# Performance work log

Measured on AMD Instinct MI355X. Metric: run time of the kernel, lower is better.

## Reference

```python
import jax, jax.numpy as jnp
import numpy as np

B, H, W, D, L, M = 16, 256, 256, 32, 4, 12  # batch, grid H, grid W, d_model, num_layers, modes
BN_EPS = 1e-5


def setup_inputs() -> dict:
    key = jax.random.key(0)
    ks = jax.random.split(key, 12)
    scale = 1.0 / (D * D)  # SpectralConv2d init scale: 1/(in_ch*out_ch)
    return {
        "x": jax.random.normal(ks[0], (B, H, W), jnp.float32),
        "coords_x": jax.random.uniform(ks[1], (1, 2, 1, H, W), dtype=jnp.float32),
        # linear_in: 3 -> D
        "w_in": jax.random.normal(ks[2], (D, 3), jnp.float32) * 0.3,
        "b_in": jnp.zeros((D,), jnp.float32),
        # per-layer spectral weights (real/imag), torch.rand-style uniform [0,1)*scale
        "w1r": jax.random.uniform(ks[3], (L, D, D, M, M), dtype=jnp.float32) * scale,
        "w1i": jax.random.uniform(ks[4], (L, D, D, M, M), dtype=jnp.float32) * scale,
        "w2r": jax.random.uniform(ks[5], (L, D, D, M, M), dtype=jnp.float32) * scale,
        "w2i": jax.random.uniform(ks[6], (L, D, D, M, M), dtype=jnp.float32) * scale,
        # per-layer pointwise linear D -> D
        "lw": jax.random.normal(ks[7], (L, D, D), jnp.float32) * (1.0 / np.sqrt(D)),
        "lb": jnp.zeros((L, D), jnp.float32),
        # per-layer BatchNorm affine params
        "gamma": jnp.ones((L, D), jnp.float32),
        "beta": jnp.zeros((L, D), jnp.float32),
        # linear_out: D -> 1
        "w_out": jax.random.normal(ks[8], (1, D), jnp.float32) * (1.0 / np.sqrt(D)),
        "b_out": jnp.zeros((1,), jnp.float32),
    }


def _fourier_layer(h, w1, w2, lw, lb, gamma, beta):
    # h: [B, D, H, W]
    Bh, C, Hh, Wh = h.shape
    h_ft = jnp.fft.rfft2(h)  # [B, D, H, W//2+1] complex64
    # low-mode truncation + complex channel mixing on two corner blocks
    top = jnp.einsum('bixy,ioxy->boxy', h_ft[:, :, :M, :M], w1)
    bot = jnp.einsum('bixy,ioxy->boxy', h_ft[:, :, Hh - M:, :M], w2)
    out_ft = jnp.zeros((Bh, C, Hh, Wh // 2 + 1), jnp.complex64)
    out_ft = out_ft.at[:, :, :M, :M].set(top).at[:, :, Hh - M:, :M].set(bot)
    y = jnp.fft.irfft2(out_ft, s=(Hh, Wh))  # [B, D, H, W]
    # residual pointwise linear (x + Linear(x)), then ReLU, then BatchNorm2d (batch stats)
    y = y + jnp.einsum('bchw,oc->bohw', y, lw) + lb[None, :, None, None]
    y = jax.nn.relu(y)
    mean = y.mean(axis=(0, 2, 3), keepdims=True)
    var = y.var(axis=(0, 2, 3), keepdims=True)
    y = (y - mean) * jax.lax.rsqrt(var + BN_EPS)
    return y * gamma[None, :, None, None] + beta[None, :, None, None]


def reference(x, coords_x, w_in, b_in, w1r, w1i, w2r, w2i, lw, lb, gamma, beta, w_out, b_out):
    # coords_x: [1,2,1,H,W] -> squeeze dim 2 -> broadcast to [B,2,H,W]
    cx = jnp.broadcast_to(coords_x[:, :, 0], (x.shape[0], 2, H, W))
    h = jnp.concatenate([x[:, None], cx], axis=1)  # [B, 3, H, W]
    h = jnp.einsum('bchw,dc->bdhw', h, w_in) + b_in[None, :, None, None]  # linear_in
    for i in range(L):  # fixed small layer count
        h = _fourier_layer(h, w1r[i] + 1j * w1i[i], w2r[i] + 1j * w2i[i],
                           lw[i], lb[i], gamma[i], beta[i])
    out = jnp.einsum('bdhw,od->bohw', h, w_out) + b_out[None, :, None, None]  # linear_out
    return out[:, 0]  # [B, H, W]
```

## Files before the change

kernel.cpp:

```cpp
#include <hip/hip_runtime.h>

constexpr double PI2 = 6.283185307179586476925286766559;
constexpr float INV_HW = 1.0f / 65536.0f;


__global__ __launch_bounds__(256) void k_init(float* __restrict__ cs,
                                              float* __restrict__ Tg) {
  int t = threadIdx.x;
  double a = PI2 * (double)t / 256.0;
  cs[2*t]   = (float)cos(a);
  cs[2*t+1] = (float)sin(a);
  for (int i = t; i < 1536; i += 256) {
    int k = i >> 7, xs = i & 127;
    double ang = PI2 * (double)(k * xs) / 256.0;
    Tg[i]        = (float)cos(ang);
    Tg[1536 + i] = (float)sin(ang);
  }
}

__global__ __launch_bounds__(256) void k_prep(
    const float* __restrict__ w1r, const float* __restrict__ w1i,
    const float* __restrict__ w2r, const float* __restrict__ w2i,
    const float* __restrict__ lw, float* __restrict__ wf)
{
  const int bid = blockIdx.x;
  const int l = bid / 288, m = bid % 288;
  const int ky = m / 12, kx = m % 12;
  const int kyp = (ky < 12) ? ky : ky - 12;
  const float* wr_ = ((ky < 12) ? w1r : w2r) + l*147456;
  const float* wi_ = ((ky < 12) ? w1i : w2i) + l*147456;
  __shared__ float wre[1024], wim[1024], lwl[1024];
  const int tid = threadIdx.x;
  for (int f = tid; f < 1024; f += 256) {
    int idx = f*144 + kyp*12 + kx;
    wre[f] = wr_[idx]; wim[f] = wi_[idx];
    lwl[f] = lw[l*1024 + f];
  }
  __syncthreads();
  float* o_ = wf + (long)bid*2048;
  for (int f = tid; f < 1024; f += 256) {
    int i = f >> 5, o = f & 31;
    float ar = wre[f], ai = wim[f];
    #pragma unroll
    for (int c = 0; c < 32; ++c) {
      float lv = lwl[o*32 + c];
      ar += wre[i*32 + c] * lv;
      ai += wim[i*32 + c] * lv;
    }
    o_[f] = ar; o_[1024 + f] = ai;
  }
}

__global__ __launch_bounds__(256) void k_embed_fwd(
    const float* __restrict__ xin, const float* __restrict__ coords,
    const float* __restrict__ w_in, const float* __restrict__ b_in,
    const float* __restrict__ Tg, float* __restrict__ gxo)
{
  __shared__ float wl[96], bl[32];
  __shared__ __align__(16) float Tl[3168];
  __shared__ __align__(16) float E[32*132];
  __shared__ __align__(16) float O[32*132];
  const int tid = threadIdx.x;
  if (tid < 96) wl[tid] = w_in[tid];
  if (tid >= 96 && tid < 128) bl[tid-96] = b_in[tid-96];
  for (int i = tid; i < 1536; i += 256) {
    int k = i >> 7, xs0 = i & 127;
    Tl[k*132 + xs0]        = Tg[i];
    Tl[1584 + k*132 + xs0] = Tg[1536 + i];
  }
  const int b = blockIdx.x >> 8, y = blockIdx.x & 255;
  const int xs = tid & 127, half = tid >> 7;
  const int cbase = half << 4;
  const int xhi = (256 - xs) & 255;
  const float xvL = xin[(b*256 + y)*256 + xs];
  const float c0L = coords[y*256 + xs];
  const float c1L = coords[65536 + y*256 + xs];
  const float xvH = xin[(b*256 + y)*256 + xhi];
  const float c0H = coords[y*256 + xhi];
  const float c1H = coords[65536 + y*256 + xhi];
  __syncthreads();
  #pragma unroll
  for (int cc = 0; cc < 16; ++cc) {
    const int c = cbase + cc;
    float lo = wl[3*c]*xvL + wl[3*c+1]*c0L + wl[3*c+2]*c1L + bl[c];
    float hi = wl[3*c]*xvH + wl[3*c+1]*c0H + wl[3*c+2]*c1H + bl[c];
    E[c*132 + xs] = (xs == 0) ? lo : (lo + hi);
    O[c*132 + xs] = (xs == 0) ? 0.f : (lo - hi);
  }
  if (tid < 32) {
    const int c = tid;
    const float xv = xin[(b*256 + y)*256 + 128];
    const float c0 = coords[y*256 + 128];
    const float c1 = coords[65536 + y*256 + 128];
    E[c*132 + 128] = wl[3*c]*xv + wl[3*c+1]*c0 + wl[3*c+2]*c1 + bl[c];
  }
  __syncthreads();
  const int wv = tid >> 6, lane = tid & 63;
  const int seg = lane >> 3, chl = lane & 7;
  const int ch = wv*8 + chl;
  float ar[12], ai[12];
  #pragma unroll
  for (int k = 0; k < 12; ++k) { ar[k] = 0.f; ai[k] = 0.f; }
  {
    const float* Erow = &E[ch*132 + seg*16];
    const float* Orow = &O[ch*132 + seg*16];
    #pragma unroll
    for (int c4 = 0; c4 < 4; ++c4) {
      float4 E4 = *(const float4*)(Erow + 4*c4);
      float4 O4 = *(const float4*)(Orow + 4*c4);
      ar[0] += E4.x + E4.y + E4.z + E4.w;
      #pragma unroll
      for (int k = 1; k < 12; ++k) {
        float4 Tc4 = *(const float4*)&Tl[k*132 + seg*16 + 4*c4];
        float4 Ts4 = *(const float4*)&Tl[1584 + k*132 + seg*16 + 4*c4];
        ar[k] += E4.x*Tc4.x + E4.y*Tc4.y + E4.z*Tc4.z + E4.w*Tc4.w;
        ai[k] -= O4.x*Ts4.x + O4.y*Ts4.y + O4.z*Ts4.z + O4.w*Ts4.w;
      }
    }
  }
  #pragma unroll
  for (int k = 0; k < 12; ++k) {
    ar[k] += __shfl_xor(ar[k], 8, 64);
    ar[k] += __shfl_xor(ar[k], 16, 64);
    ar[k] += __shfl_xor(ar[k], 32, 64);
  }
  #pragma unroll
  for (int k = 1; k < 12; ++k) {
    ai[k] += __shfl_xor(ai[k], 8, 64);
    ai[k] += __shfl_xor(ai[k], 16, 64);
    ai[k] += __shfl_xor(ai[k], 32, 64);
  }
  {
    const float e128 = E[ch*132 + 128];
    float* gp = gxo + ((long)(b*256 + y)*32 + ch)*24;
    #pragma unroll
    for (int j = 0; j < 3; ++j) {
      const int v = seg*3 + j;
      if (v < 12) {
        float s = ar[v] + ((v & 1) ? -e128 : e128);
        gp[2*v] = s;
        if (v == 0) gp[1] = 0.f;
      } else if (v < 23) {
        gp[2*(v - 11) + 1] = ai[v - 11];
      }
    }
  }
}

__global__ __launch_bounds__(512) void k_spec(
    const float* __restrict__ gx, const float* __restrict__ cs,
    const float* __restrict__ bnp, const float* __restrict__ wfl,
    float* __restrict__ gy)
{
  const int bid = (blockIdx.x % 8) * 24 + blockIdx.x / 8;
  const int b = bid / 12, kx = bid % 12;
  __shared__ float2 Z[32*257];
  __shared__ float fcl[24*66];
  __shared__ float fml[24*66];
  __shared__ __align__(16) float csl[512];
  const int tid = threadIdx.x;
  if (tid < 512) csl[tid] = cs[tid];
  {
    const int ch = tid & 31;
    float sc = 1.0f, badd = 0.0f;
    if (bnp) { sc = bnp[ch]; if (kx == 0) badd = 256.0f * bnp[32 + ch]; }
    const float* src = gx + ((long)(b*256)*32 + ch)*24 + 2*kx;
    const int ybase = tid >> 5;
    #pragma unroll
    for (int i = 0; i < 16; ++i) {
      int y = ybase + 16*i;
      float2 v = *(const float2*)(src + (long)y*768);
      float2 w; w.x = sc*v.x + badd; w.y = sc*v.y;
      Z[ch*257 + y] = w;
    }
  }
  __syncthreads();
  for (int t = tid; t < 832; t += 512) {
    const int hf = t & 1, r = t >> 1;
    const int pr = r % 13, ch = r / 13;
    const int kyv = (pr <= 10) ? (pr + 1) : ((pr == 11) ? 0 : 244);
    const int y0 = hf << 7;
    int tt = (kyv * y0) & 255;
    float A = 0.f, Bv = 0.f, C2 = 0.f, D = 0.f;
    const float2* Zp = &Z[ch*257 + y0];
    for (int i = 0; i < 128; ++i) {
      float2 v = Zp[i];
      float2 w = *(const float2*)&csl[2*tt];
      A  += v.x*w.x;  D  += v.x*w.y;
      C2 += v.y*w.x;  Bv += v.y*w.y;
      tt = (tt + kyv) & 255;
    }
    A  += __shfl_xor(A, 1, 64);
    Bv += __shfl_xor(Bv, 1, 64);
    C2 += __shfl_xor(C2, 1, 64);
    D  += __shfl_xor(D, 1, 64);
    if (hf == 0) {
      const int slo = (pr <= 10) ? (pr + 1) : ((pr == 11) ? 0 : 12);
      fcl[slo*66 + 2*ch]     = A + Bv;
      fcl[slo*66 + 2*ch + 1] = C2 - D;
      if (pr <= 10) {
        fcl[(23 - pr)*66 + 2*ch]     = A - Bv;
        fcl[(23 - pr)*66 + 2*ch + 1] = C2 + D;
      }
    }
  }
  __syncthreads();
  for (int t = tid; t < 768; t += 512) {
    const int ky = t >> 5, o = t & 31;
    const float* wb = wfl + ((long)(ky*12 + kx))*2048;
    const float* fr = &fcl[ky*66];
    float ar = 0.f, ai = 0.f;
    #pragma unroll
    for (int i = 0; i < 32; ++i) {
      float fre = fr[2*i], fim = fr[2*i+1];
      float wr = wb[i*32 + o], wi = wb[1024 + i*32 + o];
      ar += fre*wr - fim*wi;
      ai += fre*wi + fim*wr;
    }
    fml[ky*66 + 2*o]     = ar;
    fml[ky*66 + 2*o + 1] = ai;
  }
  __syncthreads();
  {
    const int yp = tid & 127, og = tid >> 7;
    float tc[24], tsn[24];
    #pragma unroll
    for (int s = 0; s < 24; ++s) {
      int kyv = (s < 12) ? s : (232 + s);
      int tt = (kyv * yp) & 255;
      tc[s] = csl[2*tt]; tsn[s] = csl[2*tt+1];
    }
    const int yhi = (256 - yp) & 255;
    float* rowLo = gy + ((long)(b*256 + yp))*768 + kx*64;
    float* rowHi = gy + ((long)(b*256 + yhi))*768 + kx*64;
    #pragma unroll
    for (int oo = 0; oo < 8; oo += 2) {
      const int o = og*8 + oo;
      float A1a=0.f,A2a=0.f,A3a=0.f,A4a=0.f;
      float A1b=0.f,A2b=0.f,A3b=0.f,A4b=0.f;
      #pragma unroll
      for (int s = 0; s < 24; ++s) {
        float fra = fml[s*66 + 2*o],     fia = fml[s*66 + 2*o + 1];
        float frb = fml[s*66 + 2*o + 2], fib = fml[s*66 + 2*o + 3];
        float c = tc[s], sn = tsn[s];
        A1a += fra*c;  A2a += fia*sn;  A3a += fra*sn;  A4a += fia*c;
        A1b += frb*c;  A2b += fib*sn;  A3b += frb*sn;  A4b += fib*c;
      }
      float4 lo, hi;
      lo.x = (A1a - A2a)*INV_HW; lo.y = (A3a + A4a)*INV_HW;
      lo.z = (A1b - A2b)*INV_HW; lo.w = (A3b + A4b)*INV_HW;
      hi.x = (A1a + A2a)*INV_HW; hi.y = (A4a - A3a)*INV_HW;
      hi.z = (A1b + A2b)*INV_HW; hi.w = (A4b - A3b)*INV_HW;
      *(float4*)(rowLo + 2*o) = lo;
      *(float4*)(rowHi + 2*o) = hi;
    }
  }
  if (tid < 32) {
    const int o = tid;
    float re = 0.f, im = 0.f;
    #pragma unroll
    for (int s = 0; s < 24; ++s) {
      float fr = fml[s*66 + 2*o], fi = fml[s*66 + 2*o + 1];
      if (s & 1) { re -= fr; im -= fi; } else { re += fr; im += fi; }
    }
    float* row = gy + ((long)(b*256 + 128))*768 + kx*64;
    row[2*o]     = re*INV_HW;
    row[2*o + 1] = im*INV_HW;
  }
}

__global__ __launch_bounds__(256) void k_fuse(
    const float* __restrict__ gy, const float* __restrict__ Tg,
    const float* __restrict__ lb,
    float* __restrict__ gxo, float* __restrict__ part, float* __restrict__ z)
{
  const int b = blockIdx.x >> 8, y = blockIdx.x & 255;
  const int tid = threadIdx.x;
  __shared__ __align__(16) float Tl[3168];
  __shared__ __align__(16) float E[32*132];
  __shared__ __align__(16) float O[32*132];
  for (int i = tid; i < 1536; i += 256) {
    int k = i >> 7, xs0 = i & 127;
    Tl[k*132 + xs0]        = Tg[i];
    Tl[1584 + k*132 + xs0] = Tg[1536 + i];
  }
  const int xs = tid & 127, half = tid >> 7;
  const int cbase = half << 4;
  const int xhi = (256 - xs) & 255;
  float tc[12], tsn[12];
  #pragma unroll
  for (int kx = 1; kx < 12; ++kx) {
    tc[kx]  = 2.0f * Tg[kx*128 + xs];
    tsn[kx] = 2.0f * Tg[1536 + kx*128 + xs];
  }
  const float* Gg = gy + (long)(b*256 + y)*768;
  float zlo[16], zhi[16];
  #pragma unroll
  for (int cc = 0; cc < 16; cc += 2) {
    const int c = cbase + cc;
    float base0 = Gg[2*c], base1 = Gg[2*c + 2];
    float cos0 = 0.f, sin0 = 0.f, cos1 = 0.f, sin1 = 0.f;
    #pragma unroll
    for (int kx = 1; kx < 12; ++kx) {
      float4 g = *(const float4*)(Gg + kx*64 + 2*c);
      cos0 += g.x*tc[kx];  sin0 += g.y*tsn[kx];
      cos1 += g.z*tc[kx];  sin1 += g.w*tsn[kx];
    }
    const float l0 = lb[c], l1 = lb[c+1];
    zlo[cc]   = fmaxf(base0 + cos0 - sin0 + l0, 0.f);
    zhi[cc]   = fmaxf(base0 + cos0 + sin0 + l0, 0.f);
    zlo[cc+1] = fmaxf(base1 + cos1 - sin1 + l1, 0.f);
    zhi[cc+1] = fmaxf(base1 + cos1 + sin1 + l1, 0.f);
  }
  #pragma unroll
  for (int cc = 0; cc < 16; ++cc) {
    float e = (xs == 0) ? zlo[cc] : (zlo[cc] + zhi[cc]);
    float o = (xs == 0) ? 0.f     : (zlo[cc] - zhi[cc]);
    E[(cbase+cc)*132 + xs] = e;
    O[(cbase+cc)*132 + xs] = o;
  }
  if (z) {
    #pragma unroll
    for (int cc = 0; cc < 16; ++cc) {
      z[((b*32 + cbase+cc)*256 + y)*256 + xs]  = zlo[cc];
      z[((b*32 + cbase+cc)*256 + y)*256 + xhi] = zhi[cc];
    }
  }
  if (tid < 32) {
    const int c = tid;
    float acc = Gg[2*c] + lb[c];
    #pragma unroll
    for (int kx = 1; kx < 12; ++kx) {
      float2 g = *(const float2*)(Gg + kx*64 + 2*c);
      acc += (kx & 1) ? (-2.0f * g.x) : (2.0f * g.x);
    }
    float zv = fmaxf(acc, 0.f);
    E[c*132 + 128] = zv;
    if (z) z[((b*32 + c)*256 + y)*256 + 128] = zv;
  }
  __syncthreads();
  const int wv = tid >> 6, lane = tid & 63;
  const int seg = lane >> 3, chl = lane & 7;
  const int ch = wv*8 + chl;
  float ar[12], ai[12], sq = 0.f;
  #pragma unroll
  for (int k = 0; k < 12; ++k) { ar[k] = 0.f; ai[k] = 0.f; }
  {
    const float* Erow = &E[ch*132 + seg*16];
    const float* Orow = &O[ch*132 + seg*16];
    if (gxo) {
      #pragma unroll
      for (int c4 = 0; c4 < 4; ++c4) {
        float4 E4 = *(const float4*)(Erow + 4*c4);
        float4 O4 = *(const float4*)(Orow + 4*c4);
        ar[0] += E4.x + E4.y + E4.z + E4.w;
        #pragma unroll
        for (int k = 1; k < 12; ++k) {
          float4 Tc4 = *(const float4*)&Tl[k*132 + seg*16 + 4*c4];
          float4 Ts4 = *(const float4*)&Tl[1584 + k*132 + seg*16 + 4*c4];
          ar[k] += E4.x*Tc4.x + E4.y*Tc4.y + E4.z*Tc4.z + E4.w*Tc4.w;
          ai[k] -= O4.x*Ts4.x + O4.y*Ts4.y + O4.z*Ts4.z + O4.w*Ts4.w;
        }
        sq += E4.x*E4.x + E4.y*E4.y + E4.z*E4.z + E4.w*E4.w
            + O4.x*O4.x + O4.y*O4.y + O4.z*O4.z + O4.w*O4.w;
      }
    } else {
      #pragma unroll
      for (int c4 = 0; c4 < 4; ++c4) {
        float4 E4 = *(const float4*)(Erow + 4*c4);
        float4 O4 = *(const float4*)(Orow + 4*c4);
        ar[0] += E4.x + E4.y + E4.z + E4.w;
        sq += E4.x*E4.x + E4.y*E4.y + E4.z*E4.z + E4.w*E4.w
            + O4.x*O4.x + O4.y*O4.y + O4.z*O4.z + O4.w*O4.w;
      }
    }
  }
  #pragma unroll
  for (int k = 0; k < 12; ++k) {
    ar[k] += __shfl_xor(ar[k], 8, 64);
    ar[k] += __shfl_xor(ar[k], 16, 64);
    ar[k] += __shfl_xor(ar[k], 32, 64);
  }
  if (gxo) {
    #pragma unroll
    for (int k = 1; k < 12; ++k) {
      ai[k] += __shfl_xor(ai[k], 8, 64);
      ai[k] += __shfl_xor(ai[k], 16, 64);
      ai[k] += __shfl_xor(ai[k], 32, 64);
    }
  }
  sq += __shfl_xor(sq, 8, 64);
  sq += __shfl_xor(sq, 16, 64);
  sq += __shfl_xor(sq, 32, 64);
  {
    const float e0   = E[ch*132];
    const float e128 = E[ch*132 + 128];
    float* gp = gxo ? (gxo + ((long)(b*256 + y)*32 + ch)*24) : nullptr;
    #pragma unroll
    for (int j = 0; j < 3; ++j) {
      const int v = seg*3 + j;
      if (v < 12) {
        float s = ar[v] + ((v & 1) ? -e128 : e128);
        if (gp) {
          gp[2*v] = s;
          if (v == 0) gp[1] = 0.f;
        }
        if (v == 0) part[(long)blockIdx.x*64 + 2*ch] = s;
      } else if (v < 23) {
        if (gp) gp[2*(v - 11) + 1] = ai[v - 11];
      } else {
        part[(long)blockIdx.x*64 + 2*ch + 1] = 0.5f*sq + 0.5f*e0*e0 + e128*e128;
      }
    }
  }
}

__global__ __launch_bounds__(256) void k_stats(
    const float* __restrict__ part, const float* __restrict__ gamma,
    const float* __restrict__ beta, float* __restrict__ bn)
{
  const int c = blockIdx.x, tid = threadIdx.x;
  float s1 = 0.f, s2 = 0.f;
  for (int j = tid; j < 4096; j += 256) {
    s1 += part[(long)j*64 + 2*c];
    s2 += part[(long)j*64 + 2*c + 1];
  }
  #pragma unroll
  for (int d = 32; d; d >>= 1) {
    s1 += __shfl_xor(s1, d, 64);
    s2 += __shfl_xor(s2, d, 64);
  }
  __shared__ float r1[4], r2[4];
  int w = tid >> 6;
  if ((tid & 63) == 0) { r1[w] = s1; r2[w] = s2; }
  __syncthreads();
  if (tid == 0) {
    float S1 = r1[0]+r1[1]+r1[2]+r1[3];
    float S2 = r2[0]+r2[1]+r2[2]+r2[3];
    const float N = 1048576.0f;
    float mean = S1 / N;
    float var  = S2 / N - mean*mean;
    float inv  = rsqrtf(var + 1e-5f);
    float sc   = gamma[c] * inv;
    bn[c]      = sc;
    bn[32 + c] = beta[c] - mean*sc;
  }
}

__global__ __launch_bounds__(256) void k_out(
    const float* __restrict__ z, const float* __restrict__ bn,
    const float* __restrict__ w_out, const float* __restrict__ b_out,
    float* __restrict__ out)
{
  __shared__ float a[32];
  __shared__ float c0s;
  const int tid = threadIdx.x;
  if (tid < 32) a[tid] = bn[tid] * w_out[tid];
  if (tid == 0) {
    float t = b_out[0];
    for (int c = 0; c < 32; ++c) t += bn[32 + c] * w_out[c];
    c0s = t;
  }
  __syncthreads();
  int gid = blockIdx.x*256 + tid;
  int b = gid >> 14, pos = (gid & 16383) << 2;
  const float* zb = z + (long)b*2097152 + pos;
  float c0 = c0s;
  float r0 = c0, r1 = c0, r2 = c0, r3 = c0;
  #pragma unroll 8
  for (int c = 0; c < 32; ++c) {
    float4 v = *(const float4*)(zb + c*65536);
    float ac = a[c];
    r0 += v.x*ac; r1 += v.y*ac; r2 += v.z*ac; r3 += v.w*ac;
  }
  float4 res; res.x = r0; res.y = r1; res.z = r2; res.w = r3;
  *(float4*)(out + (long)b*65536 + pos) = res;
}

extern "C" void kernel_launch(void* const* d_in, const int* in_sizes, int n_in,
                              void* d_out, int out_size, void* d_ws, size_t ws_size,
                              hipStream_t stream) {
  const float* x      = (const float*)d_in[0];
  const float* coords = (const float*)d_in[1];
  const float* w_in   = (const float*)d_in[2];
  const float* b_in   = (const float*)d_in[3];
  const float* w1r    = (const float*)d_in[4];
  const float* w1i    = (const float*)d_in[5];
  const float* w2r    = (const float*)d_in[6];
  const float* w2i    = (const float*)d_in[7];
  const float* lw     = (const float*)d_in[8];
  const float* lb     = (const float*)d_in[9];
  const float* gamma  = (const float*)d_in[10];
  const float* beta   = (const float*)d_in[11];
  const float* w_out  = (const float*)d_in[12];
  const float* b_out  = (const float*)d_in[13];
  float* out = (float*)d_out;
  float* ws  = (float*)d_ws;

  float* cs   = ws;
  float* z    = cs + 512;
  float* gx   = z;
  float* wf   = z + 3145728;
  float* gy   = z + 33554432;
  float* part = gy + 3145728;
  float* Tg   = part + 294912;
  float* bn   = Tg + 294912;

  k_init<<<1, 256, 0, stream>>>(cs, Tg);
  k_prep<<<1152, 256, 0, stream>>>(w1r, w1i, w2r, w2i, lw, wf);
  k_embed_fwd<<<4096, 256, 0, stream>>>(x, coords, w_in, b_in, Tg, gx);

  for (int l = 0; l < 4; ++l) {
    k_spec<<<192, 512, 0, stream>>>(gx, cs, (l == 0) ? nullptr : bn,
                                    wf + (long)l*589824, gy);
    k_fuse<<<4096, 256, 0, stream>>>(gy, Tg, lb + l*32,
                                     (l < 3) ? gx : nullptr, part,
                                     (l == 3) ? z : nullptr);
    k_stats<<<32, 256, 0, stream>>>(part, gamma + l*32, beta + l*32, bn);
  }

  k_out<<<1024, 256, 0, stream>>>(z, bn, w_out, b_out, out);
}
```

Before: 544.3 us.

## Factor the per-segment DFT twiddles and drop the shared twiddle table in k_fuse

```diff
diff --git a/kernel.cpp b/kernel.cpp
--- a/kernel.cpp
+++ b/kernel.cpp
@@ -15,6 +15,12 @@
     double ang = PI2 * (double)(k * xs) / 256.0;
     Tg[i]        = (float)cos(ang);
     Tg[1536 + i] = (float)sin(ang);
+  }
+  for (int i = t; i < 176; i += 256) {
+    int k = (i >> 4) + 1, j = i & 15;
+    double ang = PI2 * (double)(k * j) / 256.0;
+    Tg[3072 + i] = (float)cos(ang);
+    Tg[3248 + i] = (float)sin(ang);
   }
 }
 
@@ -276,14 +282,8 @@
 {
   const int b = blockIdx.x >> 8, y = blockIdx.x & 255;
   const int tid = threadIdx.x;
-  __shared__ __align__(16) float Tl[3168];
   __shared__ __align__(16) float E[32*132];
   __shared__ __align__(16) float O[32*132];
-  for (int i = tid; i < 1536; i += 256) {
-    int k = i >> 7, xs0 = i & 127;
-    Tl[k*132 + xs0]        = Tg[i];
-    Tl[1584 + k*132 + xs0] = Tg[1536 + i];
-  }
   const int xs = tid & 127, half = tid >> 7;
   const int cbase = half << 4;
   const int xhi = (256 - xs) & 255;
@@ -342,51 +342,71 @@
   const int wv = tid >> 6, lane = tid & 63;
   const int seg = lane >> 3, chl = lane & 7;
   const int ch = wv*8 + chl;
-  float ar[12], ai[12], sq = 0.f;
-  #pragma unroll
-  for (int k = 0; k < 12; ++k) { ar[k] = 0.f; ai[k] = 0.f; }
-  {
-    const float* Erow = &E[ch*132 + seg*16];
-    const float* Orow = &O[ch*132 + seg*16];
-    if (gxo) {
+  const float* Erow = &E[ch*132 + seg*16];
+  const float* Orow = &O[ch*132 + seg*16];
+  float arr[12], aii[12], sq = 0.f;
+  if (gxo) {
+    const float* T2c = Tg + 3072;
+    const float* T2s = Tg + 3248;
+    float A[11], Bv[11], Cc[11], Dd[11];
+    #pragma unroll
+    for (int k = 0; k < 11; ++k) { A[k]=0.f; Bv[k]=0.f; Cc[k]=0.f; Dd[k]=0.f; }
+    float s0 = 0.f;
+    #pragma unroll
+    for (int c4 = 0; c4 < 4; ++c4) {
+      float4 E4 = *(const float4*)(Erow + 4*c4);
+      float4 O4 = *(const float4*)(Orow + 4*c4);
+      float ej[4] = {E4.x, E4.y, E4.z, E4.w};
+      float oj[4] = {O4.x, O4.y, O4.z, O4.w};
       #pragma unroll
-      for (int c4 = 0; c4 < 4; ++c4) {
-        float4 E4 = *(const float4*)(Erow + 4*c4);
-        float4 O4 = *(const float4*)(Orow + 4*c4);
-        ar[0] += E4.x + E4.y + E4.z + E4.w;
+      for (int jj = 0; jj < 4; ++jj) {
+        const int j = 4*c4 + jj;
+        const float e = ej[jj], o = oj[jj];
+        s0 += e;
+        sq += e*e + o*o;
         #pragma unroll
-        for (int k = 1; k < 12; ++k) {
-          float4 Tc4 = *(const float4*)&Tl[k*132 + seg*16 + 4*c4];
-          float4 Ts4 = *(const float4*)&Tl[1584 + k*132 + seg*16 + 4*c4];
-          ar[k] += E4.x*Tc4.x + E4.y*Tc4.y + E4.z*Tc4.z + E4.w*Tc4.w;
-          ai[k] -= O4.x*Ts4.x + O4.y*Ts4.y + O4.z*Ts4.z + O4.w*Ts4.w;
+        for (int k = 0; k < 11; ++k) {
+          const float ckj = T2c[k*16 + j];
+          const float skj = T2s[k*16 + j];
+          A[k]  += e*ckj;
+          Bv[k] += e*skj;
+          Dd[k] += o*ckj;
+          Cc[k] += o*skj;
         }
-        sq += E4.x*E4.x + E4.y*E4.y + E4.z*E4.z + E4.w*E4.w
-            + O4.x*O4.x + O4.y*O4.y + O4.z*O4.z + O4.w*O4.w;
       }
-    } else {
-      #pragma unroll
-      for (int c4 = 0; c4 < 4; ++c4) {
-        float4 E4 = *(const float4*)(Erow + 4*c4);
-        float4 O4 = *(const float4*)(Orow + 4*c4);
-        ar[0] += E4.x + E4.y + E4.z + E4.w;
-        sq += E4.x*E4.x + E4.y*E4.y + E4.z*E4.z + E4.w*E4.w
-            + O4.x*O4.x + O4.y*O4.y + O4.z*O4.z + O4.w*O4.w;
-      }
+    }
+    arr[0] = s0; aii[0] = 0.f;
+    #pragma unroll
+    for (int k = 1; k < 12; ++k) {
+      const float twc = Tg[k*128 + seg*16];
+      const float tws = Tg[1536 + k*128 + seg*16];
+      arr[k] = A[k-1]*twc - Bv[k-1]*tws;
+      aii[k] = -(Cc[k-1]*twc + Dd[k-1]*tws);
+    }
+  } else {
+    #pragma unroll
+    for (int k = 0; k < 12; ++k) { arr[k]=0.f; aii[k]=0.f; }
+    #pragma unroll
+    for (int c4 = 0; c4 < 4; ++c4) {
+      float4 E4 = *(const float4*)(Erow + 4*c4);
+      float4 O4 = *(const float4*)(Orow + 4*c4);
+      arr[0] += E4.x + E4.y + E4.z + E4.w;
+      sq += E4.x*E4.x + E4.y*E4.y + E4.z*E4.z + E4.w*E4.w
+          + O4.x*O4.x + O4.y*O4.y + O4.z*O4.z + O4.w*O4.w;
     }
   }
   #pragma unroll
   for (int k = 0; k < 12; ++k) {
-    ar[k] += __shfl_xor(ar[k], 8, 64);
-    ar[k] += __shfl_xor(ar[k], 16, 64);
-    ar[k] += __shfl_xor(ar[k], 32, 64);
+    arr[k] += __shfl_xor(arr[k], 8, 64);
+    arr[k] += __shfl_xor(arr[k], 16, 64);
+    arr[k] += __shfl_xor(arr[k], 32, 64);
   }
   if (gxo) {
     #pragma unroll
     for (int k = 1; k < 12; ++k) {
-      ai[k] += __shfl_xor(ai[k], 8, 64);
-      ai[k] += __shfl_xor(ai[k], 16, 64);
-      ai[k] += __shfl_xor(ai[k], 32, 64);
+      aii[k] += __shfl_xor(aii[k], 8, 64);
+      aii[k] += __shfl_xor(aii[k], 16, 64);
+      aii[k] += __shfl_xor(aii[k], 32, 64);
     }
   }
   sq += __shfl_xor(sq, 8, 64);
@@ -400,14 +420,14 @@
     for (int j = 0; j < 3; ++j) {
       const int v = seg*3 + j;
       if (v < 12) {
-        float s = ar[v] + ((v & 1) ? -e128 : e128);
+        float s = arr[v] + ((v & 1) ? -e128 : e128);
         if (gp) {
           gp[2*v] = s;
           if (v == 0) gp[1] = 0.f;
         }
         if (v == 0) part[(long)blockIdx.x*64 + 2*ch] = s;
       } else if (v < 23) {
-        if (gp) gp[2*(v - 11) + 1] = ai[v - 11];
+        if (gp) gp[2*(v - 11) + 1] = aii[v - 11];
       } else {
         part[(long)blockIdx.x*64 + 2*ch + 1] = 0.5f*sq + 0.5f*e0*e0 + e128*e128;
       }
```

After: 486.0 us. 1.12x faster.
